# Optimization experiments

Hardware: AMD Instinct MI355X
Metric: run time of the kernel (lower is better)

The kernel has to match this reference:

```python
import jax, jax.numpy as jnp
import numpy as np

VOCAB = 65
N_EMBD = 32
HEAD = 16
BLOCK = 8
B = 65536


def setup_inputs() -> dict:
    key = jax.random.key(0)
    ks = jax.random.split(key, 12)
    idx = jax.random.randint(ks[0], (B, BLOCK), 0, VOCAB)
    targets = jax.random.randint(ks[1], (B, BLOCK), 0, VOCAB)
    s = 0.02
    tok_emb = jax.random.normal(ks[2], (VOCAB, N_EMBD), jnp.float32) * s
    pos_emb = jax.random.normal(ks[3], (BLOCK, N_EMBD), jnp.float32) * s
    Wk = jax.random.normal(ks[4], (N_EMBD, HEAD), jnp.float32) * s
    bk = jnp.zeros((HEAD,), jnp.float32)
    Wq = jax.random.normal(ks[5], (N_EMBD, HEAD), jnp.float32) * s
    bq = jnp.zeros((HEAD,), jnp.float32)
    Wv = jax.random.normal(ks[6], (N_EMBD, HEAD), jnp.float32) * s
    bv = jnp.zeros((HEAD,), jnp.float32)
    Wlm = jax.random.normal(ks[7], (HEAD, VOCAB), jnp.float32) * s
    blm = jnp.zeros((VOCAB,), jnp.float32)
    return {"idx": idx, "targets": targets, "tok_emb": tok_emb, "pos_emb": pos_emb,
            "Wk": Wk, "bk": bk, "Wq": Wq, "bq": bq, "Wv": Wv, "bv": bv,
            "Wlm": Wlm, "blm": blm}


def reference(idx, targets, tok_emb, pos_emb, Wk, bk, Wq, bq, Wv, bv, Wlm, blm):
    Bsz, T = idx.shape
    x = tok_emb[idx] + pos_emb[None, :T, :]                  # (B,T,C)
    k = x @ Wk + bk                                          # (B,T,H)
    q = x @ Wq + bq
    wei = jnp.einsum('bth,bsh->bts', q, k) * (HEAD ** -0.5)  # (B,T,T)
    tril = jnp.tril(jnp.ones((T, T), bool))
    wei = jnp.where(tril[None], wei, -jnp.inf)
    # NOTE: original torch code uses F.softmax(wei, dim=1) — over the QUERY axis.
    wei = jax.nn.softmax(wei, axis=1)
    v = x @ Wv + bv
    attn = jnp.einsum('bts,bsh->bth', wei, v)                # (B,T,H)
    logits = attn @ Wlm + blm                                # (B,T,V)
    logits_flat = logits.reshape(Bsz * T, VOCAB)
    tgt_flat = targets.reshape(Bsz * T)
    logp = jax.nn.log_softmax(logits_flat, axis=-1)
    loss = -jnp.mean(jnp.take_along_axis(logp, tgt_flat[:, None], axis=-1))
    return logits_flat, loss
```

## Files before the change

### kernel.cpp

```cpp
#include <hip/hip_runtime.h>
#include <hip/hip_bf16.h>

#define NVOC 65
#define NE   32
#define HD   16
#define NB   65536
#define NROWS (NB * 8)
#define NLOG  (NROWS * NVOC)


static __device__ __forceinline__ float readlane_f(float v, int l) {
  return __uint_as_float(__builtin_amdgcn_readlane(__float_as_uint(v), l));
}

__global__ __launch_bounds__(1024) void bigram_tables(
    const float* __restrict__ tok, const float* __restrict__ pos,
    const float* __restrict__ Wk, const float* __restrict__ bk,
    const float* __restrict__ Wq, const float* __restrict__ bq,
    const float* __restrict__ Wv, const float* __restrict__ bv,
    const float* __restrict__ Wlm, float* __restrict__ ws)
{
  __shared__ float S[8416];
  const int tid = threadIdx.x;
  if (tid == 0) ws[0] = 0.f;
  for (int o = tid; o < 2080; o += 1024) S[o] = tok[o];
  for (int o = tid; o < 256;  o += 1024) S[2080 + o] = pos[o];
  for (int o = tid; o < 512;  o += 1024) {
    S[2336 + o] = Wq[o]; S[2848 + o] = Wk[o]; S[3360 + o] = Wv[o];
  }
  for (int o = tid; o < 1040; o += 1024) S[3872 + o] = Wlm[o];
  __syncthreads();

  for (int o = tid; o < 1168; o += 1024) {
    if (o < 1040) {
      const int a = o >> 4, h = o & 15;
      float sq = 0.f, sk = 0.f, sv = 0.f;
      #pragma unroll
      for (int c = 0; c < NE; ++c) {
        const float e = S[a*32 + c];
        sq = fmaf(e, S[2336 + c*16 + h], sq);
        sk = fmaf(e, S[2848 + c*16 + h], sk);
        sv = fmaf(e, S[3360 + c*16 + h], sv);
      }
      S[4912 + o] = sq; S[5952 + o] = sk; S[6992 + o] = sv;
    } else {
      const int o2 = o - 1040, t = o2 >> 4, h = o2 & 15;
      float sq = bq[h], sk = bk[h], sv = bv[h];
      #pragma unroll
      for (int c = 0; c < NE; ++c) {
        const float e = S[2080 + t*32 + c];
        sq = fmaf(e, S[2336 + c*16 + h], sq);
        sk = fmaf(e, S[2848 + c*16 + h], sk);
        sv = fmaf(e, S[3360 + c*16 + h], sv);
      }
      S[8032 + o2] = sq; S[8160 + o2] = sk; S[8288 + o2] = sv;
    }
  }
  __syncthreads();

  float* wsTab = ws + 16;
  for (int o = tid; o < 10074; o += 1024) {
    float r = 0.f; int dst;
    if (o < 4225) {
      const int a = o / 65, b = o % 65;
      #pragma unroll
      for (int h = 0; h < HD; ++h) r = fmaf(S[4912 + a*16 + h], S[5952 + b*16 + h], r);
      r *= 0.25f; dst = o;
    } else if (o < 4745) {
      const int o2 = o - 4225, a = o2 >> 3, s2 = o2 & 7;
      #pragma unroll
      for (int h = 0; h < HD; ++h) r = fmaf(S[4912 + a*16 + h], S[8160 + s2*16 + h], r);
      r *= 0.25f; dst = 8450 + o2;
    } else if (o < 5265) {
      const int o2 = o - 4745, t2 = o2 / 65, b = o2 % 65;
      #pragma unroll
      for (int h = 0; h < HD; ++h) r = fmaf(S[8032 + t2*16 + h], S[5952 + b*16 + h], r);
      r *= 0.25f; dst = 8970 + o2;
    } else if (o < 5329) {
      const int o2 = o - 5265, t2 = o2 >> 3, s2 = o2 & 7;
      #pragma unroll
      for (int h = 0; h < HD; ++h) r = fmaf(S[8032 + t2*16 + h], S[8160 + s2*16 + h], r);
      r *= 0.25f; dst = 9490 + o2;
    } else if (o < 9554) {
      const int o2 = o - 5329, a = o2 / 65, j = o2 % 65;
      #pragma unroll
      for (int h = 0; h < HD; ++h) r = fmaf(S[6992 + a*16 + h], S[3872 + h*65 + j], r);
      dst = 4225 + o2;
    } else {
      const int o2 = o - 9554, s2 = o2 / 65, j = o2 % 65;
      #pragma unroll
      for (int h = 0; h < HD; ++h) r = fmaf(S[8288 + s2*16 + h], S[3872 + h*65 + j], r);
      dst = o;
    }
    wsTab[dst] = r;
  }
}

__global__ __launch_bounds__(512, 6) void bigram_main(
    const int* __restrict__ idx, const int* __restrict__ tgt,
    const float* __restrict__ blm, const float* __restrict__ ws,
    float* __restrict__ wsacc, float* __restrict__ out)
{
  __shared__ __align__(16) float S[10074];
  __shared__ float red[8];
  const int tid = threadIdx.x;
  const float* wsTab = ws + 16;
  {
    const float4* t4 = (const float4*)wsTab;
    float4* s4 = (float4*)S;
    for (int o = tid; o < 2518; o += 512) s4[o] = t4[o];
    if (tid < 2) S[10072 + tid] = wsTab[10072 + tid];
  }
  const int lane = tid & 63;
  const int w    = tid >> 6;
  const int t    = lane >> 3;
  const int s    = lane & 7;
  const float blmj  = blm[lane];
  const float blm64 = blm[64];
  const int gw = blockIdx.x * 8 + w;
  const int iv = idx[gw*64 + lane];
  const int tv = tgt[gw*64 + lane];
  __syncthreads();

  const float g4 = S[9490 + lane];
  float pvl[8], pvl64[8];
  #pragma unroll
  for (int k = 0; k < 8; ++k) {
    pvl[k]   = S[9554 + k*65 + lane];
    pvl64[k] = S[9554 + k*65 + 64];
  }

  float acc_lsm = 0.f, acc_tl = 0.f;
  for (int itb = 0; itb < 8; ++itb) {
    const int base = itb * 8;
    const int av  = __shfl(iv, base + s);
    const int a_t = __shfl(iv, base + t);
    float wr = S[a_t*65 + av] + S[8450 + a_t*8 + s] + S[8970 + t*65 + av] + g4;
    float e = (t >= s) ? __expf(wr) : 0.f;
    float sm = e;
    sm += __shfl_xor(sm, 8); sm += __shfl_xor(sm, 16); sm += __shfl_xor(sm, 32);
    const float wsm = __fdividef(e, sm);
    float Ms[8], Ms64[8];
    #pragma unroll
    for (int k = 0; k < 8; ++k) {
      const int ak = __builtin_amdgcn_readlane(iv, base + k);
      Ms[k]   = S[4225 + ak*65 + lane] + pvl[k];
      Ms64[k] = S[4225 + ak*65 + 64]  + pvl64[k];
    }
    const int rowbase = (gw*8 + itb) * 520;
    float ee[8];
    #pragma unroll
    for (int tt = 0; tt < 8; ++tt) {
      float lg = blmj, lg64 = blm64;
      #pragma unroll
      for (int k = 0; k < 8; ++k) {
        const float wk = readlane_f(wsm, tt*8 + k);
        lg   = fmaf(wk, Ms[k],   lg);
        lg64 = fmaf(wk, Ms64[k], lg64);
      }
      out[rowbase + tt*65 + lane] = lg;
      if (lane == 63) out[rowbase + tt*65 + 64] = lg64;
      float x = __expf(lg);
      if (lane == 63) x += __expf(lg64);
      ee[tt] = x;
      const int tg  = __builtin_amdgcn_readlane(tv, base + tt);
      const int tgc = tg < 64 ? tg : 0;
      const float l_at_tg = readlane_f(lg, tgc);
      acc_tl += (tg < 64) ? l_at_tg : lg64;
    }
    #pragma unroll
    for (int tt = 0; tt < 8; ++tt) {
      ee[tt] += __shfl_xor(ee[tt], 1);
      ee[tt] += __shfl_xor(ee[tt], 2);
      ee[tt] += __shfl_xor(ee[tt], 4);
    }
    const int u = lane & 7;
    float r01 = (u & 1) ? ee[1] : ee[0];
    float r23 = (u & 1) ? ee[3] : ee[2];
    float r45 = (u & 1) ? ee[5] : ee[4];
    float r67 = (u & 1) ? ee[7] : ee[6];
    float r03 = (u & 2) ? r23 : r01;
    float r47 = (u & 2) ? r67 : r45;
    float r   = (u & 4) ? r47 : r03;
    r += __shfl_xor(r, 8); r += __shfl_xor(r, 16); r += __shfl_xor(r, 32);
    acc_lsm += __logf(r);
  }
  float v = acc_lsm * 0.125f - acc_tl * 0.015625f;
  v += __shfl_xor(v, 1); v += __shfl_xor(v, 2);  v += __shfl_xor(v, 4);
  v += __shfl_xor(v, 8); v += __shfl_xor(v, 16); v += __shfl_xor(v, 32);
  if (lane == 0) red[w] = v;
  __syncthreads();
  if (tid == 0) {
    float acc = red[0] + red[1] + red[2] + red[3] + red[4] + red[5] + red[6] + red[7];
    atomicAdd(wsacc, acc);
  }
}

__global__ void bigram_fin(const float* __restrict__ ws, float* __restrict__ out) {
  if (threadIdx.x == 0) out[NLOG] = ws[0] * (1.0f / (float)NROWS);
}

extern "C" void kernel_launch(void* const* d_in, const int* in_sizes, int n_in,
                              void* d_out, int out_size, void* d_ws, size_t ws_size,
                              hipStream_t stream) {
  const int* idx = (const int*)d_in[0];
  const int* tgt = (const int*)d_in[1];
  float* ws = (float*)d_ws;
  float* out = (float*)d_out;

  bigram_tables<<<1, 1024, 0, stream>>>((const float*)d_in[2], (const float*)d_in[3],
                                        (const float*)d_in[4], (const float*)d_in[5],
                                        (const float*)d_in[6], (const float*)d_in[7],
                                        (const float*)d_in[8], (const float*)d_in[9],
                                        (const float*)d_in[10], ws);
  bigram_main<<<1024, 512, 0, stream>>>(idx, tgt, (const float*)d_in[11], ws, ws, out);
  bigram_fin<<<1, 1, 0, stream>>>(ws, out);
}
```

Baseline: 208.5 us.

## Compute vocab column 64 once per row, replace atomic with per-block partials

Column 64 of each logit row is now computed once per query position, on lanes 0-7 via shuffles, instead of being accumulated redundantly in every lane of the inner loop. Its exp is added only on those lanes. The global atomicAdd is replaced by per-block partial sums written to workspace and reduced by a 1024-thread final kernel, which also removes the need to zero the accumulator. Launch bounds are raised to 8 waves per SIMD and the index/target loads are hoisted before the shared-table copy. Together these cut ALU work and atomic contention, at the cost of possible register pressure from the tighter occupancy bound.

```diff
diff --git a/kernel.cpp b/kernel.cpp
--- a/kernel.cpp
+++ b/kernel.cpp
@@ -1,5 +1,4 @@
 #include <hip/hip_runtime.h>
-#include <hip/hip_bf16.h>
 
 #define NVOC 65
 #define NE   32
@@ -22,7 +21,6 @@
 {
   __shared__ float S[8416];
   const int tid = threadIdx.x;
-  if (tid == 0) ws[0] = 0.f;
   for (int o = tid; o < 2080; o += 1024) S[o] = tok[o];
   for (int o = tid; o < 256;  o += 1024) S[2080 + o] = pos[o];
   for (int o = tid; o < 512;  o += 1024) {
@@ -96,14 +94,24 @@
   }
 }
 
-__global__ __launch_bounds__(512, 6) void bigram_main(
+__global__ __launch_bounds__(512, 8) void bigram_main(
     const int* __restrict__ idx, const int* __restrict__ tgt,
     const float* __restrict__ blm, const float* __restrict__ ws,
-    float* __restrict__ wsacc, float* __restrict__ out)
+    float* __restrict__ wsout, float* __restrict__ out)
 {
   __shared__ __align__(16) float S[10074];
   __shared__ float red[8];
   const int tid = threadIdx.x;
+  const int lane = tid & 63;
+  const int w    = tid >> 6;
+  const int t    = lane >> 3;
+  const int s    = lane & 7;
+  const int u    = lane & 7;
+  const int gw = blockIdx.x * 8 + w;
+  const int iv = idx[gw*64 + lane];
+  const int tv = tgt[gw*64 + lane];
+  const float blmj  = blm[lane];
+  const float blm64 = blm[64];
   const float* wsTab = ws + 16;
   {
     const float4* t4 = (const float4*)wsTab;
@@ -111,15 +119,6 @@
     for (int o = tid; o < 2518; o += 512) s4[o] = t4[o];
     if (tid < 2) S[10072 + tid] = wsTab[10072 + tid];
   }
-  const int lane = tid & 63;
-  const int w    = tid >> 6;
-  const int t    = lane >> 3;
-  const int s    = lane & 7;
-  const float blmj  = blm[lane];
-  const float blm64 = blm[64];
-  const int gw = blockIdx.x * 8 + w;
-  const int iv = idx[gw*64 + lane];
-  const int tv = tgt[gw*64 + lane];
   __syncthreads();
 
   const float g4 = S[9490 + lane];
@@ -147,26 +146,30 @@
       Ms[k]   = S[4225 + ak*65 + lane] + pvl[k];
       Ms64[k] = S[4225 + ak*65 + 64]  + pvl64[k];
     }
+    float lg64v = blm64;
+    #pragma unroll
+    for (int k = 0; k < 8; ++k) {
+      const float wk_row = __shfl(wsm, u*8 + k);
+      lg64v = fmaf(wk_row, Ms64[k], lg64v);
+    }
     const int rowbase = (gw*8 + itb) * 520;
+    if (lane < 8) out[rowbase + lane*65 + 64] = lg64v;
     float ee[8];
     #pragma unroll
     for (int tt = 0; tt < 8; ++tt) {
-      float lg = blmj, lg64 = blm64;
+      float lg = blmj;
       #pragma unroll
       for (int k = 0; k < 8; ++k) {
         const float wk = readlane_f(wsm, tt*8 + k);
-        lg   = fmaf(wk, Ms[k],   lg);
-        lg64 = fmaf(wk, Ms64[k], lg64);
+        lg = fmaf(wk, Ms[k], lg);
       }
       out[rowbase + tt*65 + lane] = lg;
-      if (lane == 63) out[rowbase + tt*65 + 64] = lg64;
-      float x = __expf(lg);
-      if (lane == 63) x += __expf(lg64);
-      ee[tt] = x;
+      ee[tt] = __expf(lg);
       const int tg  = __builtin_amdgcn_readlane(tv, base + tt);
       const int tgc = tg < 64 ? tg : 0;
       const float l_at_tg = readlane_f(lg, tgc);
-      acc_tl += (tg < 64) ? l_at_tg : lg64;
+      const float l64t    = readlane_f(lg64v, tt);
+      acc_tl += (tg < 64) ? l_at_tg : l64t;
     }
     #pragma unroll
     for (int tt = 0; tt < 8; ++tt) {
@@ -174,7 +177,6 @@
       ee[tt] += __shfl_xor(ee[tt], 2);
       ee[tt] += __shfl_xor(ee[tt], 4);
     }
-    const int u = lane & 7;
     float r01 = (u & 1) ? ee[1] : ee[0];
     float r23 = (u & 1) ? ee[3] : ee[2];
     float r45 = (u & 1) ? ee[5] : ee[4];
@@ -182,6 +184,7 @@
     float r03 = (u & 2) ? r23 : r01;
     float r47 = (u & 2) ? r67 : r45;
     float r   = (u & 4) ? r47 : r03;
+    if (lane < 8) r += __expf(lg64v);
     r += __shfl_xor(r, 8); r += __shfl_xor(r, 16); r += __shfl_xor(r, 32);
     acc_lsm += __logf(r);
   }
@@ -191,13 +194,27 @@
   if (lane == 0) red[w] = v;
   __syncthreads();
   if (tid == 0) {
-    float acc = red[0] + red[1] + red[2] + red[3] + red[4] + red[5] + red[6] + red[7];
-    atomicAdd(wsacc, acc);
-  }
-}
-
-__global__ void bigram_fin(const float* __restrict__ ws, float* __restrict__ out) {
-  if (threadIdx.x == 0) out[NLOG] = ws[0] * (1.0f / (float)NROWS);
+    wsout[10112 + blockIdx.x] = red[0] + red[1] + red[2] + red[3]
+                              + red[4] + red[5] + red[6] + red[7];
+  }
+}
+
+__global__ __launch_bounds__(1024) void bigram_fin2(
+    const float* __restrict__ ws, float* __restrict__ out)
+{
+  __shared__ float r[16];
+  const int tid = threadIdx.x;
+  float v = ws[10112 + tid];
+  v += __shfl_xor(v, 1); v += __shfl_xor(v, 2);  v += __shfl_xor(v, 4);
+  v += __shfl_xor(v, 8); v += __shfl_xor(v, 16); v += __shfl_xor(v, 32);
+  if ((tid & 63) == 0) r[tid >> 6] = v;
+  __syncthreads();
+  if (tid == 0) {
+    float a = 0.f;
+    #pragma unroll
+    for (int i = 0; i < 16; ++i) a += r[i];
+    out[NLOG] = a * (1.0f / (float)NROWS);
+  }
 }
 
 extern "C" void kernel_launch(void* const* d_in, const int* in_sizes, int n_in,
@@ -214,5 +231,5 @@
                                         (const float*)d_in[8], (const float*)d_in[9],
                                         (const float*)d_in[10], ws);
   bigram_main<<<1024, 512, 0, stream>>>(idx, tgt, (const float*)d_in[11], ws, ws, out);
-  bigram_fin<<<1, 1, 0, stream>>>(ws, out);
-}
+  bigram_fin2<<<1, 1024, 0, stream>>>(ws, out);
+}
```

Result: faster. 200.7 us (-3.7%).
